# Performance work log

Hardware: AMD Instinct MI355X
Metric: run time of the kernel (lower is better)

## Reference

```python
import jax, jax.numpy as jnp
import numpy as np

NUM_HEADS = 12
HEAD_DIM = 64
MAX_POS = 1024  # max_position_embeddings


def setup_inputs() -> dict:
    key = jax.random.key(0)
    ks = jax.random.split(key, 6)
    B, S, H = 4, 1024, 768
    return {
        "hidden_states": jax.random.normal(ks[0], (B, S, H), dtype=jnp.float32),
        "attention_mask": jnp.zeros((B, 1, 1, S), dtype=jnp.float32),
        "Wq": jax.random.normal(ks[1], (H, H), dtype=jnp.float32) * 0.02,
        "bq": jnp.zeros((H,), dtype=jnp.float32),
        "Wk": jax.random.normal(ks[2], (H, H), dtype=jnp.float32) * 0.02,
        "bk": jnp.zeros((H,), dtype=jnp.float32),
        "Wv": jax.random.normal(ks[3], (H, H), dtype=jnp.float32) * 0.02,
        "bv": jnp.zeros((H,), dtype=jnp.float32),
        "dist_emb": jax.random.normal(ks[4], (2 * MAX_POS - 1, HEAD_DIM), dtype=jnp.float32) * 0.02,
    }


def _split_heads(x):
    # [B, S, H] -> [B, nh, S, hd]
    B, S, _ = x.shape
    return x.reshape(B, S, NUM_HEADS, HEAD_DIM).transpose(0, 2, 1, 3)


def reference(hidden_states, attention_mask, Wq, bq, Wk, bk, Wv, bv, dist_emb):
    B, S, H = hidden_states.shape
    q = _split_heads(hidden_states @ Wq + bq)  # [B, nh, S, hd]
    k = _split_heads(hidden_states @ Wk + bk)
    v = _split_heads(hidden_states @ Wv + bv)

    # raw scores QK^T: [B, nh, S, S]
    scores = jnp.einsum("bhld,bhrd->bhlr", q, k)

    # relative_key_query positional bias
    dist = jnp.arange(S)[:, None] - jnp.arange(S)[None, :] + MAX_POS - 1  # [S, S]
    pos = dist_emb[dist]  # [S, S, hd]
    scores = scores + jnp.einsum("bhld,lrd->bhlr", q, pos) \
                    + jnp.einsum("bhrd,lrd->bhlr", k, pos)

    scores = scores / jnp.sqrt(jnp.asarray(HEAD_DIM, scores.dtype))
    scores = scores + attention_mask  # additive mask broadcast [B,1,1,S]

    probs = jax.nn.softmax(scores, axis=-1)  # dropout prob = 0.0 (eval)
    ctx = jnp.einsum("bhlr,bhrd->bhld", probs, v)  # [B, nh, S, hd]
    ctx = ctx.transpose(0, 2, 1, 3).reshape(B, S, H)
    return ctx
```

## Files before the change

kernel.cpp:

```cpp
#include <hip/hip_runtime.h>

#define SEQ 1024
#define NH  12
#define HD  64
#define HID 768
#define NB  4

#define LOG2E  1.4426950408889634f
#define SC2    0.18033688011112042f
#define DTHR   11.541560327111707f

typedef short bf16x8 __attribute__((ext_vector_type(8)));
typedef float f32x16 __attribute__((ext_vector_type(16)));

#define LBAR() do {                                             \
    __builtin_amdgcn_sched_barrier(0);                          \
    asm volatile("s_waitcnt lgkmcnt(0)" ::: "memory");          \
    __builtin_amdgcn_s_barrier();                               \
    __builtin_amdgcn_sched_barrier(0);                          \
} while (0)

__device__ __forceinline__ unsigned short f2b(float f) {
    union { float f; unsigned u; } v; v.f = f;
    unsigned r = (v.u + 0x7FFFu + ((v.u >> 16) & 1u)) >> 16;
    return (unsigned short)r;
}
__device__ __forceinline__ float b2f(unsigned short s) {
    union { unsigned u; float f; } v; v.u = (unsigned)s << 16;
    return v.f;
}
__device__ __forceinline__ float g4(const float4& v, int e) {
    return e == 0 ? v.x : e == 1 ? v.y : e == 2 ? v.z : v.w;
}
__device__ __forceinline__ unsigned short u16g(const ushort4& v, int e) {
    return e == 0 ? v.x : e == 1 ? v.y : e == 2 ? v.z : v.w;
}

#define ROWFN(r, h) (((r) & 3) + 8 * ((r) >> 2) + 4 * (h))

__global__ void cvt_bf16(const float* __restrict__ in, unsigned short* __restrict__ outp, int n4) {
    int i = blockIdx.x * blockDim.x + threadIdx.x;
    const int stride = gridDim.x * blockDim.x;
    for (; i < n4; i += stride) {
        float4 v = ((const float4*)in)[i];
        ushort4 o;
        o.x = f2b(v.x); o.y = f2b(v.y); o.z = f2b(v.z); o.w = f2b(v.w);
        ((ushort4*)outp)[i] = o;
    }
}

__global__ __launch_bounds__(256) void cvt_wt(
    const float* __restrict__ Wq, const float* __restrict__ Wk, const float* __restrict__ Wv,
    unsigned short* __restrict__ Wt)
{
    __shared__ float T[64][65];
    const int z = blockIdx.z;
    const float* __restrict__ W = (z == 0) ? Wq : (z == 1) ? Wk : Wv;
    const int k0 = blockIdx.x * 64, n0 = blockIdx.y * 64;
    const int tid = threadIdx.x;
    #pragma unroll
    for (int ir = 0; ir < 4; ++ir) {
        int r = ir * 16 + (tid >> 4);
        int c4 = (tid & 15) * 4;
        *(float4*)&T[r][c4] = *(const float4*)&W[(size_t)(k0 + r) * HID + n0 + c4];
    }
    __syncthreads();
    const int cc = tid >> 2, q = tid & 3;
    unsigned short* dst = Wt + (size_t)z * HID * HID + (size_t)(n0 + cc) * HID + k0 + q * 16;
    #pragma unroll
    for (int j4 = 0; j4 < 4; ++j4) {
        ushort4 t4;
        t4.x = f2b(T[q * 16 + j4 * 4 + 0][cc]);
        t4.y = f2b(T[q * 16 + j4 * 4 + 1][cc]);
        t4.z = f2b(T[q * 16 + j4 * 4 + 2][cc]);
        t4.w = f2b(T[q * 16 + j4 * 4 + 3][cc]);
        *(ushort4*)(dst + j4 * 4) = t4;
    }
}

__global__ __launch_bounds__(256) void gemm_qkv(
    const unsigned short* __restrict__ Xb,
    const unsigned short* __restrict__ Wt,
    const float* __restrict__ bq, const float* __restrict__ bk, const float* __restrict__ bv,
    unsigned short* __restrict__ qkv)
{
    __shared__ unsigned short Xs[128][64];
    __shared__ unsigned short Ws[128][64];

    const int tid = threadIdx.x;
    const int lane = tid & 63;
    const int wid = tid >> 6;
    const int c = lane & 31;
    const int h2 = lane >> 5;
    const int m0 = blockIdx.x * 128, N0 = blockIdx.y * 128, z = blockIdx.z;
    const unsigned short* __restrict__ Wz = Wt + (size_t)z * HID * HID;
    const float* __restrict__ bias = (z == 0) ? bq : (z == 1) ? bk : bv;

    f32x16 acc[2][2];
    #pragma unroll
    for (int i = 0; i < 2; ++i)
        #pragma unroll
        for (int j = 0; j < 2; ++j)
            #pragma unroll
            for (int r = 0; r < 16; ++r) acc[i][j][r] = 0.f;

    for (int k0 = 0; k0 < HID; k0 += 64) {
        __syncthreads();
        #pragma unroll
        for (int it = 0; it < 4; ++it) {
            int t16 = tid + 256 * it;
            int row = t16 >> 3, s = t16 & 7;
            bf16x8 xv = *(const bf16x8*)(Xb + (size_t)(m0 + row) * HID + k0 + s * 8);
            *(bf16x8*)&Xs[row][(s ^ (row & 7)) * 8] = xv;
            bf16x8 wv = *(const bf16x8*)(Wz + (size_t)(N0 + row) * HID + k0 + s * 8);
            *(bf16x8*)&Ws[row][(s ^ (row & 7)) * 8] = wv;
        }
        __syncthreads();
        #pragma unroll
        for (int kc = 0; kc < 4; ++kc) {
            const int slot = kc * 2 + h2;
            bf16x8 af[2], bf_[2];
            #pragma unroll
            for (int i = 0; i < 2; ++i) {
                int ar = 64 * (wid >> 1) + 32 * i + c;
                int br = 64 * (wid & 1) + 32 * i + c;
                if (z != 2) {
                    af[i]  = *(const bf16x8*)&Xs[ar][(slot ^ (ar & 7)) * 8];
                    bf_[i] = *(const bf16x8*)&Ws[br][(slot ^ (br & 7)) * 8];
                } else {
                    af[i]  = *(const bf16x8*)&Ws[ar][(slot ^ (ar & 7)) * 8];
                    bf_[i] = *(const bf16x8*)&Xs[br][(slot ^ (br & 7)) * 8];
                }
            }
            #pragma unroll
            for (int i = 0; i < 2; ++i)
                #pragma unroll
                for (int j = 0; j < 2; ++j)
                    acc[i][j] = __builtin_amdgcn_mfma_f32_32x32x16_bf16(af[i], bf_[j], acc[i][j], 0, 0, 0);
        }
    }

    unsigned short* outz = qkv + (size_t)z * (NB * SEQ * HID);
    if (z != 2) {
        #pragma unroll
        for (int j = 0; j < 2; ++j) {
            const int n = N0 + 64 * (wid & 1) + 32 * j + c;
            const float bv_ = bias[n];
            const int hh = n >> 6, d = n & 63;
            #pragma unroll
            for (int i = 0; i < 2; ++i) {
                #pragma unroll
                for (int r = 0; r < 16; ++r) {
                    int m = m0 + 64 * (wid >> 1) + 32 * i + ROWFN(r, h2);
                    int bb = m >> 10, ss = m & 1023;
                    outz[(((size_t)bb * NH + hh) * SEQ + ss) * HD + d] = f2b(acc[i][j][r] + bv_);
                }
            }
        }
    } else {
        #pragma unroll
        for (int i = 0; i < 2; ++i) {
            #pragma unroll
            for (int r = 0; r < 16; ++r) {
                int n = N0 + 64 * (wid >> 1) + 32 * i + ROWFN(r, h2);
                float bv_ = bias[n];
                int hh = n >> 6, d = n & 63;
                #pragma unroll
                for (int j = 0; j < 2; ++j) {
                    int m = m0 + 64 * (wid & 1) + 32 * j + c;
                    int bb = m >> 10, ss = m & 1023;
                    outz[(((size_t)bb * NH + hh) * HD + d) * SEQ + ss] = f2b(acc[i][j][r] + bv_);
                }
            }
        }
    }
}

__global__ __launch_bounds__(256, 2) void attn_mfma(
    const unsigned short* __restrict__ Qg,
    const unsigned short* __restrict__ Kg,
    const unsigned short* __restrict__ Vtg,
    const unsigned short* __restrict__ Eg,
    const float* __restrict__ mask,
    float* __restrict__ out)
{
    __shared__ unsigned short Vt[64][64];
    __shared__ float S1[64][68];
    __shared__ unsigned short MSS[64][76];
    __shared__ unsigned short NST[64][76];
    __shared__ unsigned short Pl[64][64];
    __shared__ float Corr[64];
    __shared__ float InvL[64];

    const int tid = threadIdx.x;
    const int lane = tid & 63;
    const int wid = tid >> 6;
    const int c = lane & 31;
    const int h2 = lane >> 5;
    const int RB = 32 * (wid >> 1);
    const int CB = 32 * (wid & 1);
    const int j0 = 64 * (wid & 1) + c;

    const int l0 = blockIdx.x * 64;
    const int bh = blockIdx.y;
    const int b = bh / NH;
    const int hh = bh - b * NH;

    const unsigned short* __restrict__ Qb = Qg + (size_t)bh * SEQ * HD;
    const unsigned short* __restrict__ Kb = Kg + (size_t)bh * SEQ * HD;
    const unsigned short* __restrict__ Vb = Vtg + (size_t)bh * HD * SEQ;
    const float* __restrict__ mrow_base = mask + (size_t)b * SEQ;

    bf16x8 qa[4];
    #pragma unroll
    for (int kc = 0; kc < 4; ++kc)
        qa[kc] = *(const bf16x8*)(Qb + (size_t)(l0 + RB + c) * HD + kc * 16 + h2 * 8);

    f32x16 Oa;
    #pragma unroll
    for (int r = 0; r < 16; ++r) Oa[r] = 0.f;

    const int li = tid >> 2;
    const int c0q = (tid & 3) * 16;
    const int kli = (li ^ (li >> 3)) & 7;
    const int vd0 = tid >> 3, vs8 = tid & 7;
    const int kd0 = (vd0 ^ (vd0 >> 3)) & 7;
    const int kd1 = ((vd0 + 32) ^ ((vd0 + 32) >> 3)) & 7;
    float m_run = -1e30f, lsum = 0.f;

    bf16x8 kb[4], ka[4], e0[4], e1[4], vc0, vc1;
    {
        const int jr0 = l0 + 960 + j0;
        const int jra = jr0 > 2046 ? 2046 : jr0;
        const int jr1x = jr0 + 32;
        const int jrb = jr1x > 2046 ? 2046 : jr1x;
        #pragma unroll
        for (int kc = 0; kc < 4; ++kc) {
            kb[kc] = *(const bf16x8*)(Kb + (size_t)(CB + c) * HD + kc * 16 + h2 * 8);
            ka[kc] = *(const bf16x8*)(Kb + (size_t)(RB + c) * HD + kc * 16 + h2 * 8);
            e0[kc] = *(const bf16x8*)(Eg + (size_t)jra * HD + kc * 16 + h2 * 8);
            e1[kc] = *(const bf16x8*)(Eg + (size_t)jrb * HD + kc * 16 + h2 * 8);
        }
        vc0 = *(const bf16x8*)(Vb + (size_t)vd0 * SEQ + vs8 * 8);
        vc1 = *(const bf16x8*)(Vb + (size_t)(vd0 + 32) * SEQ + vs8 * 8);
    }

    for (int r0 = 0; r0 < SEQ; r0 += 64) {
        int r0n = r0 + 64; if (r0n >= SEQ) r0n = 0;

        float4 mk[4];
        #pragma unroll
        for (int q = 0; q < 4; ++q)
            mk[q] = *(const float4*)(mrow_base + r0 + c0q + 4 * q);

        {
            f32x16 s1a;
            #pragma unroll
            for (int r = 0; r < 16; ++r) s1a[r] = 0.f;
            __builtin_amdgcn_s_setprio(1);
            #pragma unroll
            for (int kc = 0; kc < 4; ++kc)
                s1a = __builtin_amdgcn_mfma_f32_32x32x16_bf16(qa[kc], kb[kc], s1a, 0, 0, 0);
            __builtin_amdgcn_s_setprio(0);
            #pragma unroll
            for (int rq = 0; rq < 16; ++rq)
                S1[RB + ROWFN(rq, h2)][CB + c] = s1a[rq];
        }
        #pragma unroll
        for (int kc = 0; kc < 4; ++kc)
            kb[kc] = *(const bf16x8*)(Kb + (size_t)(r0n + CB + c) * HD + kc * 16 + h2 * 8);
        __builtin_amdgcn_sched_barrier(0);

        {
            f32x16 ma0, na0;
            #pragma unroll
            for (int r = 0; r < 16; ++r) { ma0[r] = 0.f; na0[r] = 0.f; }
            __builtin_amdgcn_s_setprio(1);
            #pragma unroll
            for (int kc = 0; kc < 4; ++kc) {
                ma0 = __builtin_amdgcn_mfma_f32_32x32x16_bf16(qa[kc], e0[kc], ma0, 0, 0, 0);
                na0 = __builtin_amdgcn_mfma_f32_32x32x16_bf16(ka[kc], e0[kc], na0, 0, 0, 0);
            }
            __builtin_amdgcn_s_setprio(0);
            #pragma unroll
            for (int rq = 0; rq < 16; ++rq) {
                const int lr = RB + ROWFN(rq, h2);
                int rA = lr - j0 + 63;
                if ((unsigned)rA < 64u) MSS[lr][rA] = f2b(ma0[rq]);
                int lA = j0 + lr - 63;
                if ((unsigned)lA < 64u) NST[lA][lr] = f2b(na0[rq]);
            }
        }
        __builtin_amdgcn_sched_barrier(0);

        {
            f32x16 ma1, na1;
            #pragma unroll
            for (int r = 0; r < 16; ++r) { ma1[r] = 0.f; na1[r] = 0.f; }
            __builtin_amdgcn_s_setprio(1);
            #pragma unroll
            for (int kc = 0; kc < 4; ++kc) {
                ma1 = __builtin_amdgcn_mfma_f32_32x32x16_bf16(qa[kc], e1[kc], ma1, 0, 0, 0);
                na1 = __builtin_amdgcn_mfma_f32_32x32x16_bf16(ka[kc], e1[kc], na1, 0, 0, 0);
            }
            __builtin_amdgcn_s_setprio(0);
            #pragma unroll
            for (int rq = 0; rq < 16; ++rq) {
                const int lr = RB + ROWFN(rq, h2);
                int rB = lr - j0 + 31;
                if ((unsigned)rB < 64u) MSS[lr][rB] = f2b(ma1[rq]);
                int lB = j0 + lr - 31;
                if ((unsigned)lB < 64u) NST[lB][lr] = f2b(na1[rq]);
            }
        }

        bf16x8 vn0, vn1;
        {
            const int jr0n = l0 - r0n + 960 + j0;
            const int jran = jr0n > 2046 ? 2046 : jr0n;
            const int jr1n = jr0n + 32;
            const int jrbn = jr1n > 2046 ? 2046 : jr1n;
            #pragma unroll
            for (int kc = 0; kc < 4; ++kc) {
                ka[kc] = *(const bf16x8*)(Kb + (size_t)(r0n + RB + c) * HD + kc * 16 + h2 * 8);
                e0[kc] = *(const bf16x8*)(Eg + (size_t)jran * HD + kc * 16 + h2 * 8);
                e1[kc] = *(const bf16x8*)(Eg + (size_t)jrbn * HD + kc * 16 + h2 * 8);
            }
            vn0 = *(const bf16x8*)(Vb + (size_t)vd0 * SEQ + r0n + vs8 * 8);
            vn1 = *(const bf16x8*)(Vb + (size_t)(vd0 + 32) * SEQ + r0n + vs8 * 8);
        }

        LBAR();

        *(bf16x8*)&Vt[vd0][(vs8 ^ kd0) * 8] = vc0;
        *(bf16x8*)&Vt[vd0 + 32][(vs8 ^ kd1) * 8] = vc1;

        float4 s4[4]; ushort4 mm[4], nn[4];
        #pragma unroll
        for (int q = 0; q < 4; ++q) {
            s4[q] = *(const float4*)&S1[li][c0q + 4 * q];
            mm[q] = *(const ushort4*)&MSS[li][c0q + 4 * q];
            nn[q] = *(const ushort4*)&NST[li][c0q + 4 * q];
        }
        float sc[16];
        #pragma unroll
        for (int j = 0; j < 16; ++j) {
            float mv = b2f(u16g(mm[j >> 2], j & 3));
            float nv = b2f(u16g(nn[j >> 2], j & 3));
            sc[j] = (g4(s4[j >> 2], j & 3) + mv + nv) * SC2 + g4(mk[j >> 2], j & 3) * LOG2E;
        }
        float tmax = sc[0];
        #pragma unroll
        for (int j = 1; j < 16; ++j) tmax = fmaxf(tmax, sc[j]);
        tmax = fmaxf(tmax, __shfl_xor(tmax, 1));
        tmax = fmaxf(tmax, __shfl_xor(tmax, 2));
        const bool upd = tmax > m_run + DTHR;
        const float m_new = upd ? tmax : m_run;
        const float corr = upd ? __builtin_amdgcn_exp2f(m_run - m_new) : 1.0f;
        float tsum = 0.f;
        unsigned short pb[16];
        #pragma unroll
        for (int j = 0; j < 16; ++j) {
            float p = __builtin_amdgcn_exp2f(sc[j] - m_new);
            tsum += p;
            pb[j] = f2b(p);
        }
        tsum += __shfl_xor(tsum, 1);
        tsum += __shfl_xor(tsum, 2);
        lsum = lsum * corr + tsum;
        m_run = m_new;
        if ((tid & 3) == 0) Corr[li] = corr;
        #pragma unroll
        for (int sblk = 0; sblk < 2; ++sblk) {
            bf16x8 pv;
            #pragma unroll
            for (int e = 0; e < 8; ++e) pv[e] = (short)pb[sblk * 8 + e];
            const int slot = ((c0q >> 3) + sblk) ^ kli;
            *(bf16x8*)&Pl[li][slot * 8] = pv;
        }

        LBAR();

        #pragma unroll
        for (int q = 0; q < 4; ++q) {
            float4 cr = *(const float4*)&Corr[RB + 8 * q + 4 * h2];
            Oa[4 * q + 0] *= cr.x; Oa[4 * q + 1] *= cr.y;
            Oa[4 * q + 2] *= cr.z; Oa[4 * q + 3] *= cr.w;
        }
        const int lrow = RB + c;
        const int drow = CB + c;
        const int klr = (lrow ^ (lrow >> 3)) & 7;
        const int kdr = (drow ^ (drow >> 3)) & 7;
        __builtin_amdgcn_s_setprio(1);
        #pragma unroll
        for (int kc = 0; kc < 4; ++kc) {
            const int slot = kc * 2 + h2;
            bf16x8 pa  = *(const bf16x8*)&Pl[lrow][(slot ^ klr) * 8];
            bf16x8 vbf = *(const bf16x8*)&Vt[drow][(slot ^ kdr) * 8];
            Oa = __builtin_amdgcn_mfma_f32_32x32x16_bf16(pa, vbf, Oa, 0, 0, 0);
        }
        __builtin_amdgcn_s_setprio(0);

        vc0 = vn0; vc1 = vn1;
    }

    if ((tid & 3) == 0) InvL[li] = 1.0f / lsum;
    __syncthreads();
    #pragma unroll
    for (int q = 0; q < 4; ++q) {
        float4 iv = *(const float4*)&InvL[RB + 8 * q + 4 * h2];
        #pragma unroll
        for (int e = 0; e < 4; ++e) {
            const int l = RB + 8 * q + 4 * h2 + e;
            out[((size_t)b * SEQ + l0 + l) * HID + hh * HD + CB + c] = Oa[4 * q + e] * g4(iv, e);
        }
    }
}

extern "C" void kernel_launch(void* const* d_in, const int* in_sizes, int n_in,
                              void* d_out, int out_size, void* d_ws, size_t ws_size,
                              hipStream_t stream) {
    const float* hidden = (const float*)d_in[0];
    const float* mask   = (const float*)d_in[1];
    const float* Wq     = (const float*)d_in[2];
    const float* bq     = (const float*)d_in[3];
    const float* Wk     = (const float*)d_in[4];
    const float* bk     = (const float*)d_in[5];
    const float* Wv     = (const float*)d_in[6];
    const float* bv     = (const float*)d_in[7];
    const float* E      = (const float*)d_in[8];
    float* outp = (float*)d_out;

    unsigned short* ws  = (unsigned short*)d_ws;
    unsigned short* Xbf = ws;
    unsigned short* Wt  = ws + 3145728;
    unsigned short* Ebf = ws + 4915200;
    unsigned short* qkv = ws + 5046272;

    cvt_bf16<<<dim3(1024), 256, 0, stream>>>(hidden, Xbf, 786432);
    cvt_bf16<<<dim3(128),  256, 0, stream>>>(E, Ebf, 32752);
    cvt_wt<<<dim3(12, 12, 3), 256, 0, stream>>>(Wq, Wk, Wv, Wt);
    gemm_qkv<<<dim3(32, 6, 3), 256, 0, stream>>>(Xbf, Wt, bq, bk, bv, qkv);
    const size_t per = (size_t)NB * SEQ * HID;
    attn_mfma<<<dim3(16, 48), 256, 0, stream>>>(qkv, qkv + per, qkv + 2 * per,
                                                Ebf, mask, outp);
}
```

Before: 176.8 us.

## Skip dead relative-position MFMA tiles per wave, gate rescale, fuse conversions

```diff
diff --git a/kernel.cpp b/kernel.cpp
--- a/kernel.cpp
+++ b/kernel.cpp
@@ -38,14 +38,21 @@
 
 #define ROWFN(r, h) (((r) & 3) + 8 * ((r) >> 2) + 4 * (h))
 
-__global__ void cvt_bf16(const float* __restrict__ in, unsigned short* __restrict__ outp, int n4) {
+#define NX4 786432
+#define NE4 32752
+
+__global__ void cvt_all(const float* __restrict__ X, const float* __restrict__ E,
+                        unsigned short* __restrict__ Xb, unsigned short* __restrict__ Eb) {
     int i = blockIdx.x * blockDim.x + threadIdx.x;
     const int stride = gridDim.x * blockDim.x;
-    for (; i < n4; i += stride) {
-        float4 v = ((const float4*)in)[i];
+    for (; i < NX4 + NE4; i += stride) {
+        float4 v;
+        if (i < NX4) v = ((const float4*)X)[i];
+        else         v = ((const float4*)E)[i - NX4];
         ushort4 o;
         o.x = f2b(v.x); o.y = f2b(v.y); o.z = f2b(v.z); o.w = f2b(v.w);
-        ((ushort4*)outp)[i] = o;
+        if (i < NX4) ((ushort4*)Xb)[i] = o;
+        else         ((ushort4*)Eb)[i - NX4] = o;
     }
 }
 
@@ -191,6 +198,7 @@
     __shared__ unsigned short Pl[64][64];
     __shared__ float Corr[64];
     __shared__ float InvL[64];
+    __shared__ int Fl[2];
 
     const int tid = threadIdx.x;
     const int lane = tid & 63;
@@ -211,6 +219,8 @@
     const unsigned short* __restrict__ Vb = Vtg + (size_t)bh * HD * SEQ;
     const float* __restrict__ mrow_base = mask + (size_t)b * SEQ;
 
+    if (tid < 2) Fl[tid] = 0;
+
     bf16x8 qa[4];
     #pragma unroll
     for (int kc = 0; kc < 4; ++kc)
@@ -246,6 +256,7 @@
     }
 
     for (int r0 = 0; r0 < SEQ; r0 += 64) {
+        const int buf = (r0 >> 6) & 1;
         int r0n = r0 + 64; if (r0n >= SEQ) r0n = 0;
 
         float4 mk[4];
@@ -276,19 +287,32 @@
             #pragma unroll
             for (int r = 0; r < 16; ++r) { ma0[r] = 0.f; na0[r] = 0.f; }
             __builtin_amdgcn_s_setprio(1);
-            #pragma unroll
-            for (int kc = 0; kc < 4; ++kc) {
-                ma0 = __builtin_amdgcn_mfma_f32_32x32x16_bf16(qa[kc], e0[kc], ma0, 0, 0, 0);
-                na0 = __builtin_amdgcn_mfma_f32_32x32x16_bf16(ka[kc], e0[kc], na0, 0, 0, 0);
+            if (wid != 2) {
+                #pragma unroll
+                for (int kc = 0; kc < 4; ++kc)
+                    ma0 = __builtin_amdgcn_mfma_f32_32x32x16_bf16(qa[kc], e0[kc], ma0, 0, 0, 0);
+            }
+            if (wid != 0) {
+                #pragma unroll
+                for (int kc = 0; kc < 4; ++kc)
+                    na0 = __builtin_amdgcn_mfma_f32_32x32x16_bf16(ka[kc], e0[kc], na0, 0, 0, 0);
             }
             __builtin_amdgcn_s_setprio(0);
-            #pragma unroll
-            for (int rq = 0; rq < 16; ++rq) {
-                const int lr = RB + ROWFN(rq, h2);
-                int rA = lr - j0 + 63;
-                if ((unsigned)rA < 64u) MSS[lr][rA] = f2b(ma0[rq]);
-                int lA = j0 + lr - 63;
-                if ((unsigned)lA < 64u) NST[lA][lr] = f2b(na0[rq]);
+            if (wid != 2) {
+                #pragma unroll
+                for (int rq = 0; rq < 16; ++rq) {
+                    const int lr = RB + ROWFN(rq, h2);
+                    int rA = lr - j0 + 63;
+                    if ((unsigned)rA < 64u) MSS[lr][rA] = f2b(ma0[rq]);
+                }
+            }
+            if (wid != 0) {
+                #pragma unroll
+                for (int rq = 0; rq < 16; ++rq) {
+                    const int lr = RB + ROWFN(rq, h2);
+                    int lA = j0 + lr - 63;
+                    if ((unsigned)lA < 64u) NST[lA][lr] = f2b(na0[rq]);
+                }
             }
         }
         __builtin_amdgcn_sched_barrier(0);
@@ -298,21 +322,35 @@
             #pragma unroll
             for (int r = 0; r < 16; ++r) { ma1[r] = 0.f; na1[r] = 0.f; }
             __builtin_amdgcn_s_setprio(1);
-            #pragma unroll
-            for (int kc = 0; kc < 4; ++kc) {
-                ma1 = __builtin_amdgcn_mfma_f32_32x32x16_bf16(qa[kc], e1[kc], ma1, 0, 0, 0);
-                na1 = __builtin_amdgcn_mfma_f32_32x32x16_bf16(ka[kc], e1[kc], na1, 0, 0, 0);
+            if (wid != 1) {
+                #pragma unroll
+                for (int kc = 0; kc < 4; ++kc)
+                    ma1 = __builtin_amdgcn_mfma_f32_32x32x16_bf16(qa[kc], e1[kc], ma1, 0, 0, 0);
+            }
+            if (wid != 3) {
+                #pragma unroll
+                for (int kc = 0; kc < 4; ++kc)
+                    na1 = __builtin_amdgcn_mfma_f32_32x32x16_bf16(ka[kc], e1[kc], na1, 0, 0, 0);
             }
             __builtin_amdgcn_s_setprio(0);
-            #pragma unroll
-            for (int rq = 0; rq < 16; ++rq) {
-                const int lr = RB + ROWFN(rq, h2);
-                int rB = lr - j0 + 31;
-                if ((unsigned)rB < 64u) MSS[lr][rB] = f2b(ma1[rq]);
-                int lB = j0 + lr - 31;
-                if ((unsigned)lB < 64u) NST[lB][lr] = f2b(na1[rq]);
-            }
-        }
+            if (wid != 1) {
+                #pragma unroll
+                for (int rq = 0; rq < 16; ++rq) {
+                    const int lr = RB + ROWFN(rq, h2);
+                    int rB = lr - j0 + 31;
+                    if ((unsigned)rB < 64u) MSS[lr][rB] = f2b(ma1[rq]);
+                }
+            }
+            if (wid != 3) {
+                #pragma unroll
+                for (int rq = 0; rq < 16; ++rq) {
+                    const int lr = RB + ROWFN(rq, h2);
+                    int lB = j0 + lr - 31;
+                    if ((unsigned)lB < 64u) NST[lB][lr] = f2b(na1[rq]);
+                }
+            }
+        }
+        __builtin_amdgcn_sched_barrier(0);
 
         bf16x8 vn0, vn1;
         {
@@ -357,6 +395,7 @@
         const bool upd = tmax > m_run + DTHR;
         const float m_new = upd ? tmax : m_run;
         const float corr = upd ? __builtin_amdgcn_exp2f(m_run - m_new) : 1.0f;
+        if (upd) Fl[buf] = 1;
         float tsum = 0.f;
         unsigned short pb[16];
         #pragma unroll
@@ -381,12 +420,15 @@
 
         LBAR();
 
-        #pragma unroll
-        for (int q = 0; q < 4; ++q) {
-            float4 cr = *(const float4*)&Corr[RB + 8 * q + 4 * h2];
-            Oa[4 * q + 0] *= cr.x; Oa[4 * q + 1] *= cr.y;
-            Oa[4 * q + 2] *= cr.z; Oa[4 * q + 3] *= cr.w;
-        }
+        if (Fl[buf]) {
+            #pragma unroll
+            for (int q = 0; q < 4; ++q) {
+                float4 cr = *(const float4*)&Corr[RB + 8 * q + 4 * h2];
+                Oa[4 * q + 0] *= cr.x; Oa[4 * q + 1] *= cr.y;
+                Oa[4 * q + 2] *= cr.z; Oa[4 * q + 3] *= cr.w;
+            }
+        }
+        if (tid == 0) Fl[buf ^ 1] = 0;
         const int lrow = RB + c;
         const int drow = CB + c;
         const int klr = (lrow ^ (lrow >> 3)) & 7;
@@ -437,8 +479,7 @@
     unsigned short* Ebf = ws + 4915200;
     unsigned short* qkv = ws + 5046272;
 
-    cvt_bf16<<<dim3(1024), 256, 0, stream>>>(hidden, Xbf, 786432);
-    cvt_bf16<<<dim3(128),  256, 0, stream>>>(E, Ebf, 32752);
+    cvt_all<<<dim3(1024), 256, 0, stream>>>(hidden, E, Xbf, Ebf);
     cvt_wt<<<dim3(12, 12, 3), 256, 0, stream>>>(Wq, Wk, Wv, Wt);
     gemm_qkv<<<dim3(32, 6, 3), 256, 0, stream>>>(Xbf, Wt, bq, bk, bv, qkv);
     const size_t per = (size_t)NB * SEQ * HID;
```

Measured after the change: 170.0 us. 3.8% less time.
